# Kernel optimization log

Measured on AMD Instinct MI355X. Metric: run time of the kernel, lower is better.

Reference implementation:

```python
import jax, jax.numpy as jnp
import numpy as np

N_RES = 8192
N_IN = 128
BATCH = 16
RES_NNZ = int(0.1 * N_RES * N_RES)  # 6710886
IN_NNZ = int(0.1 * N_RES * N_IN)    # 104857
LEAK = 0.9


def spmm_coo(vals, rows, cols, inputs, n_out):
    """COO SpMM: out[b, r] = sum_{n: rows[n]==r} vals[n] * inputs[b, cols[n]].
    Equivalent to (coo_matmat(vals, rows, cols, inputs.T, shape=(n_out, F)).T)."""
    contrib = vals[:, None] * inputs.T[cols]  # [nnz, B]
    return jax.ops.segment_sum(contrib, rows, num_segments=n_out).T  # [B, n_out]


def leaky_erf(z, state, a=LEAK):
    return (1.0 - a) * state + a * jax.scipy.special.erf(z)


def setup_inputs() -> dict:
    key = jax.random.key(0)
    ks = jax.random.split(key, 10)
    return {
        "state": jax.random.normal(ks[0], (BATCH, N_RES), jnp.float32),
        "x": jax.random.normal(ks[1], (BATCH, N_IN), jnp.float32),
        "res_vals": jax.random.normal(ks[2], (RES_NNZ,), jnp.float32),
        "res_rows": jax.random.randint(ks[3], (RES_NNZ,), 0, N_RES, jnp.int32),
        "res_cols": jax.random.randint(ks[4], (RES_NNZ,), 0, N_RES, jnp.int32),
        "res_bias": jax.random.normal(ks[5], (N_RES,), jnp.float32),
        "in_vals": jax.random.normal(ks[6], (IN_NNZ,), jnp.float32),
        "in_rows": jax.random.randint(ks[7], (IN_NNZ,), 0, N_RES, jnp.int32),
        "in_cols": jax.random.randint(ks[8], (IN_NNZ,), 0, N_IN, jnp.int32),
        "in_bias": jax.random.normal(ks[9], (N_RES,), jnp.float32),
    }


def reference(state, x, res_vals, res_rows, res_cols, res_bias,
              in_vals, in_rows, in_cols, in_bias):
    z_res = spmm_coo(res_vals, res_rows, res_cols, state, N_RES) + res_bias
    z_in = spmm_coo(in_vals, in_rows, in_cols, x, N_RES) + in_bias
    return leaky_erf(z_in + z_res, state)
```

## Files before the change

### kernel.cpp

```cpp
#include <hip/hip_runtime.h>
#include <math.h>

#define N_RES 8192
#define N_IN  128
#define BATCH 16
#define LEAK  0.9f

#define NBK    128
#define CAP1B  55296
#define CHUNK1 8192
#define CHUNK2 4096
#define SB2    14
#define TBLK   128


#define OFF_SRCT 0
#define OFF_BCUR (1u << 20)
#define OFF_Z    (2u << 20)
#define OFF_E1   (8u << 20)
#define REQ_A    ((size_t)OFF_E1 + (size_t)NBK * CAP1B * 8)

__global__ __launch_bounds__(1024, 8) void pass1_fused(
    const float* __restrict__ state,
    const float* __restrict__ x,
    const float* __restrict__ vres, const int* __restrict__ rres,
    const int* __restrict__ cres, int nres, int nbres,
    const float* __restrict__ vin, const int* __restrict__ rin,
    const int* __restrict__ cin, int nin, int nchunks,
    float* __restrict__ srcT,
    float* __restrict__ z,
    uint2* __restrict__ e1,
    int* __restrict__ bcur) {
  int tid = threadIdx.x;

  if (blockIdx.x >= nchunks) {
    int idx0 = (blockIdx.x - nchunks) * 1024 + tid;
    const int stride = TBLK * 1024;
    for (int i = idx0; i < N_RES * BATCH; i += stride) {
      int b = i >> 13;
      int r = i & (N_RES - 1);
      srcT[r * BATCH + b] = state[i];
      z[i] = 0.0f;
    }
    for (int i = idx0; i < N_IN * BATCH; i += stride) {
      int b = i >> 7;
      int c = i & (N_IN - 1);
      srcT[(N_RES + c) * BATCH + b] = x[i];
    }
    return;
  }

  const float* vals; const int* rows; const int* cols;
  int nnz, col_off, base;
  if (blockIdx.x < nbres) {
    vals = vres; rows = rres; cols = cres; nnz = nres; col_off = 0;
    base = blockIdx.x * CHUNK1;
  } else {
    vals = vin; rows = rin; cols = cin; nnz = nin; col_off = N_RES;
    base = (blockIdx.x - nbres) * CHUNK1;
  }

  __shared__ uint2 stg[CHUNK1];
  __shared__ int hist[NBK];
  __shared__ int lbase[NBK];
  __shared__ int gbase[NBK];
  __shared__ int wsum[2];
  int wave = tid >> 6, lane = tid & 63;

  if (tid < NBK) hist[tid] = 0;
  __syncthreads();

  int n = nnz - base;
  if (n > CHUNK1) n = CHUNK1;

  uint2 ent[8];
  int lp[8];
  unsigned msk = 0;
#pragma unroll
  for (int g = 0; g < 2; ++g) {
    int i0 = (g * 1024 + tid) * 4;
    if (i0 + 3 < n) {
      int4 r4 = *(const int4*)(rows + base + i0);
      int4 c4 = *(const int4*)(cols + base + i0);
      float4 v4 = *(const float4*)(vals + base + i0);
      int rr_[4] = {r4.x, r4.y, r4.z, r4.w};
      int cc_[4] = {c4.x, c4.y, c4.z, c4.w};
      float vv_[4] = {v4.x, v4.y, v4.z, v4.w};
#pragma unroll
      for (int j = 0; j < 4; ++j) {
        int e = g * 4 + j;
        ent[e] = make_uint2(__float_as_uint(vv_[j]),
                            ((unsigned)rr_[j] << 14) |
                                (unsigned)(cc_[j] + col_off));
        msk |= 1u << e;
        lp[e] = atomicAdd(&hist[rr_[j] >> 6], 1);
      }
    } else {
#pragma unroll
      for (int j = 0; j < 4; ++j) {
        int e = g * 4 + j, i = i0 + j;
        if (i < n) {
          int r = rows[base + i];
          int c = cols[base + i] + col_off;
          float v = vals[base + i];
          ent[e] = make_uint2(__float_as_uint(v),
                              ((unsigned)r << 14) | (unsigned)c);
          msk |= 1u << e;
          lp[e] = atomicAdd(&hist[r >> 6], 1);
        }
      }
    }
  }
  __syncthreads();

  int h = 0, v = 0;
  if (tid < NBK) {
    h = hist[tid];
    v = h;
#pragma unroll
    for (int d = 1; d < 64; d <<= 1) {
      int t = __shfl_up(v, d);
      if (lane >= d) v += t;
    }
    if (lane == 63) wsum[wave] = v;
  }
  __syncthreads();
  if (tid < NBK) {
    int off = (wave == 1) ? wsum[0] : 0;
    lbase[tid] = off + v - h;
    gbase[tid] = h ? atomicAdd(&bcur[tid], h) : 0;
  }
  __syncthreads();
#pragma unroll
  for (int e = 0; e < 8; ++e) {
    if (msk & (1u << e)) {
      int b = (int)(ent[e].y >> 20);
      stg[lbase[b] + lp[e]] = ent[e];
    }
  }
  __syncthreads();
  for (int i = tid; i < n; i += 1024) {
    uint2 ld = stg[i];
    int b = (int)(ld.y >> 20);
    int p = gbase[b] + (i - lbase[b]);
    if (p < CAP1B) e1[(size_t)b * CAP1B + p] = ld;
  }
}

__global__ __launch_bounds__(512, 8) void pass2_accum(
    const uint2* __restrict__ e1,
    const int* __restrict__ bcur,
    const float* __restrict__ srcT,
    float* __restrict__ z) {
  int bucket = blockIdx.y;
  int ch = blockIdx.x;
  int tid = threadIdx.x;

  int cnt = bcur[bucket];
  if (cnt > CAP1B) cnt = CAP1B;
  int base = ch * CHUNK2;
  if (base >= cnt) return;
  int n = cnt - base;
  if (n > CHUNK2) n = CHUNK2;

  __shared__ int acc[64 * 17];
  for (int i = tid; i < 64 * 17; i += 512) acc[i] = 0;
  __syncthreads();

  const uint2* __restrict__ src = e1 + (size_t)bucket * CAP1B + base;
  int wave = tid >> 6, lane = tid & 63;
  int g = lane >> 2;
  int bq = lane & 3;
  const float4* __restrict__ s4 = (const float4*)srcT;

  int bw = wave * (CHUNK2 / 8);
  int lim = n - bw;
  if (lim > CHUNK2 / 8) lim = CHUNK2 / 8;
  for (int s = 0; s < lim; s += 32) {
    int i1 = bw + s + g;
    int i2 = bw + s + 16 + g;
    int c1 = (i1 < n) ? i1 : n - 1;
    int c2 = (i2 < n) ? i2 : n - 1;
    uint2 eA = src[c1];
    uint2 eB = src[c2];
    float4 sA = s4[(int)(eA.y & 16383u) * 4 + bq];
    float4 sB = s4[(int)(eB.y & 16383u) * 4 + bq];
    float vA = (i1 < n) ? __uint_as_float(eA.x) * 65536.f : 0.0f;
    float vB = (i2 < n) ? __uint_as_float(eB.x) * 65536.f : 0.0f;
    int aA = (int)((eA.y >> 14) & 63u) * 17 + (bq << 2);
    int aB = (int)((eB.y >> 14) & 63u) * 17 + (bq << 2);
    atomicAdd(&acc[aA + 0], __float2int_rn(vA * sA.x));
    atomicAdd(&acc[aA + 1], __float2int_rn(vA * sA.y));
    atomicAdd(&acc[aA + 2], __float2int_rn(vA * sA.z));
    atomicAdd(&acc[aA + 3], __float2int_rn(vA * sA.w));
    atomicAdd(&acc[aB + 0], __float2int_rn(vB * sB.x));
    atomicAdd(&acc[aB + 1], __float2int_rn(vB * sB.y));
    atomicAdd(&acc[aB + 2], __float2int_rn(vB * sB.z));
    atomicAdd(&acc[aB + 3], __float2int_rn(vB * sB.w));
  }
  __syncthreads();
  for (int i = tid; i < 64 * BATCH; i += 512) {
    int rr = i >> 4, b = i & 15;
    float fv = (float)acc[rr * 17 + b] * (1.0f / 65536.f);
    unsafeAtomicAdd(&z[(size_t)(bucket * 64 + rr) * BATCH + b], fv);
  }
}

__global__ __launch_bounds__(256) void finalize_z(
    const float* __restrict__ z, const float* __restrict__ state,
    const float* __restrict__ res_bias, const float* __restrict__ in_bias,
    float* __restrict__ out) {
  int tid = blockIdx.x * 256 + threadIdx.x;
  if (tid >= BATCH * N_RES) return;
  int b = tid >> 13;
  int r = tid & (N_RES - 1);
  float zz = z[r * 16 + b] + res_bias[r] + in_bias[r];
  out[tid] = (1.0f - LEAK) * state[tid] + LEAK * erff(zz);
}

__global__ __launch_bounds__(256) void transpose_nb(
    const float* __restrict__ state, const float* __restrict__ x,
    float* __restrict__ srcT) {
  int tid = blockIdx.x * 256 + threadIdx.x;
  if (tid < N_RES * BATCH) {
    int b = tid >> 13;
    int r = tid & (N_RES - 1);
    srcT[r * BATCH + b] = state[tid];
  }
  if (tid < N_IN * BATCH) {
    int b = tid >> 7;
    int c = tid & (N_IN - 1);
    srcT[(N_RES + c) * BATCH + b] = x[tid];
  }
}

__global__ __launch_bounds__(256) void spmm_atomic(
    const float* __restrict__ vals, const int* __restrict__ rows,
    const int* __restrict__ cols, const float* __restrict__ srcT,
    int col_off, float* __restrict__ zz, int nnz) {
  int i = blockIdx.x * blockDim.x + threadIdx.x;
  if (i >= nnz) return;
  float v = vals[i];
  int r = rows[i];
  int c = cols[i] + col_off;
  const float4* __restrict__ sp = (const float4*)(srcT + c * BATCH);
  float* zr = zz + r * BATCH;
#pragma unroll
  for (int qq = 0; qq < 4; ++qq) {
    float4 s = sp[qq];
    unsafeAtomicAdd(zr + qq * 4 + 0, v * s.x);
    unsafeAtomicAdd(zr + qq * 4 + 1, v * s.y);
    unsafeAtomicAdd(zr + qq * 4 + 2, v * s.z);
    unsafeAtomicAdd(zr + qq * 4 + 3, v * s.w);
  }
}

extern "C" void kernel_launch(void* const* d_in, const int* in_sizes, int n_in,
                              void* d_out, int out_size, void* d_ws, size_t ws_size,
                              hipStream_t stream) {
  const float* state    = (const float*)d_in[0];
  const float* x        = (const float*)d_in[1];
  const float* res_vals = (const float*)d_in[2];
  const int*   res_rows = (const int*)d_in[3];
  const int*   res_cols = (const int*)d_in[4];
  const float* res_bias = (const float*)d_in[5];
  const float* in_vals  = (const float*)d_in[6];
  const int*   in_rows  = (const int*)d_in[7];
  const int*   in_cols  = (const int*)d_in[8];
  const float* in_bias  = (const float*)d_in[9];

  const int res_nnz = in_sizes[2];
  const int in_nnz  = in_sizes[6];

  char* ws = (char*)d_ws;
  float* srcT = (float*)(ws + OFF_SRCT);
  float* z    = (float*)(ws + OFF_Z);
  float* out = (float*)d_out;

  if (ws_size >= REQ_A) {
    int* bcur = (int*)(ws + OFF_BCUR);
    uint2* e1 = (uint2*)(ws + OFF_E1);
    int nbres = (res_nnz + CHUNK1 - 1) / CHUNK1;
    int nbin  = (in_nnz + CHUNK1 - 1) / CHUNK1;
    int nchunks = nbres + nbin;

    hipMemsetAsync(bcur, 0, NBK * sizeof(int), stream);

    pass1_fused<<<nchunks + TBLK, 1024, 0, stream>>>(
        state, x, res_vals, res_rows, res_cols, res_nnz, nbres,
        in_vals, in_rows, in_cols, in_nnz, nchunks, srcT, z, e1, bcur);

    pass2_accum<<<dim3(SB2, NBK), 512, 0, stream>>>(e1, bcur, srcT, z);

    finalize_z<<<512, 256, 0, stream>>>(z, state, res_bias, in_bias, out);
  } else {
    hipMemsetAsync(z, 0, N_RES * BATCH * sizeof(float), stream);
    transpose_nb<<<512, 256, 0, stream>>>(state, x, srcT);
    spmm_atomic<<<(res_nnz + 255) / 256, 256, 0, stream>>>(
        res_vals, res_rows, res_cols, srcT, 0, z, res_nnz);
    spmm_atomic<<<(in_nnz + 255) / 256, 256, 0, stream>>>(
        in_vals, in_rows, in_cols, srcT, N_RES, z, in_nnz);
    finalize_z<<<512, 256, 0, stream>>>(z, state, res_bias, in_bias, out);
  }
}
```

Measured before the change: 185.9 us.

## Fuse all passes into one cooperative persistent kernel with grid syncs

Replaces the memset plus three kernel launches with a single cooperative kernel of 512 blocks that runs transpose/zero, bucket scatter, bucket accumulation and finalize as phases separated by grid-wide syncs. The goal is to remove launch gaps and the separate memset. In exchange, pass1 now runs in a grid-stride loop over chunks with fewer blocks, pass2 runs with 1024-thread blocks over a persistent loop, and three grid barriers are added. Co-residency of 512 blocks of 1024 threads must hold, otherwise the code falls back to the old path.

```diff
diff --git a/kernel.cpp b/kernel.cpp
--- a/kernel.cpp
+++ b/kernel.cpp
@@ -1,5 +1,8 @@
 #include <hip/hip_runtime.h>
+#include <hip/hip_cooperative_groups.h>
 #include <math.h>
+
+namespace cg = cooperative_groups;
 
 #define N_RES 8192
 #define N_IN  128
@@ -12,6 +15,7 @@
 #define CHUNK2 4096
 #define SB2    14
 #define TBLK   128
+#define GRID_B 512
 
 
 #define OFF_SRCT 0
@@ -20,7 +24,7 @@
 #define OFF_E1   (8u << 20)
 #define REQ_A    ((size_t)OFF_E1 + (size_t)NBK * CAP1B * 8)
 
-__global__ __launch_bounds__(1024, 8) void pass1_fused(
+__global__ __launch_bounds__(1024, 8) void fused_all(
     const float* __restrict__ state,
     const float* __restrict__ x,
     const float* __restrict__ vres, const int* __restrict__ rres,
@@ -30,7 +34,213 @@
     float* __restrict__ srcT,
     float* __restrict__ z,
     uint2* __restrict__ e1,
-    int* __restrict__ bcur) {
+    int* __restrict__ bcur,
+    const float* __restrict__ res_bias,
+    const float* __restrict__ in_bias,
+    float* __restrict__ out) {
+  cg::grid_group grid = cg::this_grid();
+  int tid = threadIdx.x;
+  int bid = blockIdx.x;
+
+  __shared__ __align__(16) char smem[CHUNK1 * 8 + 1536];
+
+  {
+    int idx = bid * 1024 + tid;
+    if (idx < N_RES * BATCH) {
+      int b = idx >> 13;
+      int r = idx & (N_RES - 1);
+      srcT[r * BATCH + b] = state[idx];
+      z[idx] = 0.0f;
+    }
+    if (idx < N_IN * BATCH) {
+      int b = idx >> 7;
+      int c = idx & (N_IN - 1);
+      srcT[(N_RES + c) * BATCH + b] = x[idx];
+    }
+    if (idx < NBK) bcur[idx] = 0;
+  }
+  grid.sync();
+
+  {
+    uint2* stg = (uint2*)smem;
+    int* hist  = (int*)(smem + CHUNK1 * 8);
+    int* lbase = (int*)(smem + CHUNK1 * 8 + 512);
+    int* gbase = (int*)(smem + CHUNK1 * 8 + 1024);
+    int* wsum  = (int*)(smem + CHUNK1 * 8 + 1528);
+    int wave = tid >> 6, lane = tid & 63;
+
+    for (int chk = bid; chk < nchunks; chk += GRID_B) {
+      const float* vals; const int* rows; const int* cols;
+      int nnz, col_off, base;
+      if (chk < nbres) {
+        vals = vres; rows = rres; cols = cres; nnz = nres; col_off = 0;
+        base = chk * CHUNK1;
+      } else {
+        vals = vin; rows = rin; cols = cin; nnz = nin; col_off = N_RES;
+        base = (chk - nbres) * CHUNK1;
+      }
+
+      if (tid < NBK) hist[tid] = 0;
+      __syncthreads();
+
+      int n = nnz - base;
+      if (n > CHUNK1) n = CHUNK1;
+
+      uint2 ent[8];
+      int lp[8];
+      unsigned msk = 0;
+#pragma unroll
+      for (int gg = 0; gg < 2; ++gg) {
+        int i0 = (gg * 1024 + tid) * 4;
+        if (i0 + 3 < n) {
+          int4 r4 = *(const int4*)(rows + base + i0);
+          int4 c4 = *(const int4*)(cols + base + i0);
+          float4 v4 = *(const float4*)(vals + base + i0);
+          int rr_[4] = {r4.x, r4.y, r4.z, r4.w};
+          int cc_[4] = {c4.x, c4.y, c4.z, c4.w};
+          float vv_[4] = {v4.x, v4.y, v4.z, v4.w};
+#pragma unroll
+          for (int j = 0; j < 4; ++j) {
+            int e = gg * 4 + j;
+            ent[e] = make_uint2(__float_as_uint(vv_[j]),
+                                ((unsigned)rr_[j] << 14) |
+                                    (unsigned)(cc_[j] + col_off));
+            msk |= 1u << e;
+            lp[e] = atomicAdd(&hist[rr_[j] >> 6], 1);
+          }
+        } else {
+#pragma unroll
+          for (int j = 0; j < 4; ++j) {
+            int e = gg * 4 + j, i = i0 + j;
+            if (i < n) {
+              int r = rows[base + i];
+              int c = cols[base + i] + col_off;
+              float v = vals[base + i];
+              ent[e] = make_uint2(__float_as_uint(v),
+                                  ((unsigned)r << 14) | (unsigned)c);
+              msk |= 1u << e;
+              lp[e] = atomicAdd(&hist[r >> 6], 1);
+            }
+          }
+        }
+      }
+      __syncthreads();
+
+      int h = 0, v = 0;
+      if (tid < NBK) {
+        h = hist[tid];
+        v = h;
+#pragma unroll
+        for (int d = 1; d < 64; d <<= 1) {
+          int t = __shfl_up(v, d);
+          if (lane >= d) v += t;
+        }
+        if (lane == 63) wsum[wave] = v;
+      }
+      __syncthreads();
+      if (tid < NBK) {
+        int off = (wave == 1) ? wsum[0] : 0;
+        lbase[tid] = off + v - h;
+        gbase[tid] = h ? atomicAdd(&bcur[tid], h) : 0;
+      }
+      __syncthreads();
+#pragma unroll
+      for (int e = 0; e < 8; ++e) {
+        if (msk & (1u << e)) {
+          int b = (int)(ent[e].y >> 20);
+          stg[lbase[b] + lp[e]] = ent[e];
+        }
+      }
+      __syncthreads();
+      for (int i = tid; i < n; i += 1024) {
+        uint2 ld = stg[i];
+        int b = (int)(ld.y >> 20);
+        int p = gbase[b] + (i - lbase[b]);
+        if (p < CAP1B) e1[(size_t)b * CAP1B + p] = ld;
+      }
+    }
+  }
+  grid.sync();
+
+  {
+    int* acc = (int*)smem;
+    int wave = tid >> 6, lane = tid & 63;
+    int g = lane >> 2;
+    int bq = lane & 3;
+    const float4* __restrict__ s4 = (const float4*)srcT;
+
+    for (int u = bid; u < SB2 * NBK; u += GRID_B) {
+      int bucket = u & (NBK - 1);
+      int ch = u >> 7;
+      int cnt = bcur[bucket];
+      if (cnt > CAP1B) cnt = CAP1B;
+      int base = ch * CHUNK2;
+      int n = cnt - base;
+      if (n < 0) n = 0;
+      if (n > CHUNK2) n = CHUNK2;
+
+      for (int i = tid; i < 64 * 17; i += 1024) acc[i] = 0;
+      __syncthreads();
+
+      if (n > 0) {
+        const uint2* __restrict__ src = e1 + (size_t)bucket * CAP1B + base;
+        int bw = wave * (CHUNK2 / 16);
+        int lim = n - bw;
+        if (lim < 0) lim = 0;
+        if (lim > CHUNK2 / 16) lim = CHUNK2 / 16;
+        for (int s = 0; s < lim; s += 32) {
+          int i1 = bw + s + g;
+          int i2 = bw + s + 16 + g;
+          int c1 = (i1 < n) ? i1 : n - 1;
+          int c2 = (i2 < n) ? i2 : n - 1;
+          uint2 eA = src[c1];
+          uint2 eB = src[c2];
+          float4 sA = s4[(int)(eA.y & 16383u) * 4 + bq];
+          float4 sB = s4[(int)(eB.y & 16383u) * 4 + bq];
+          float vA = (i1 < n) ? __uint_as_float(eA.x) * 65536.f : 0.0f;
+          float vB = (i2 < n) ? __uint_as_float(eB.x) * 65536.f : 0.0f;
+          int aA = (int)((eA.y >> 14) & 63u) * 17 + (bq << 2);
+          int aB = (int)((eB.y >> 14) & 63u) * 17 + (bq << 2);
+          atomicAdd(&acc[aA + 0], __float2int_rn(vA * sA.x));
+          atomicAdd(&acc[aA + 1], __float2int_rn(vA * sA.y));
+          atomicAdd(&acc[aA + 2], __float2int_rn(vA * sA.z));
+          atomicAdd(&acc[aA + 3], __float2int_rn(vA * sA.w));
+          atomicAdd(&acc[aB + 0], __float2int_rn(vB * sB.x));
+          atomicAdd(&acc[aB + 1], __float2int_rn(vB * sB.y));
+          atomicAdd(&acc[aB + 2], __float2int_rn(vB * sB.z));
+          atomicAdd(&acc[aB + 3], __float2int_rn(vB * sB.w));
+        }
+      }
+      __syncthreads();
+      if (n > 0 && tid < 64 * BATCH) {
+        int rr = tid >> 4, b = tid & 15;
+        float fv = (float)acc[rr * 17 + b] * (1.0f / 65536.f);
+        unsafeAtomicAdd(&z[(size_t)(bucket * 64 + rr) * BATCH + b], fv);
+      }
+      __syncthreads();
+    }
+  }
+  grid.sync();
+
+  {
+    int idx = bid * 1024 + tid;
+    if (idx < BATCH * N_RES) {
+      int b = idx >> 13;
+      int r = idx & (N_RES - 1);
+      float zz = z[r * 16 + b] + res_bias[r] + in_bias[r];
+      out[idx] = (1.0f - LEAK) * state[idx] + LEAK * erff(zz);
+    }
+  }
+}
+
+__global__ __launch_bounds__(1024, 8) void pass1_fused(
+    const float* __restrict__ state, const float* __restrict__ x,
+    const float* __restrict__ vres, const int* __restrict__ rres,
+    const int* __restrict__ cres, int nres, int nbres,
+    const float* __restrict__ vin, const int* __restrict__ rin,
+    const int* __restrict__ cin, int nin, int nchunks,
+    float* __restrict__ srcT, float* __restrict__ z,
+    uint2* __restrict__ e1, int* __restrict__ bcur) {
   int tid = threadIdx.x;
 
   if (blockIdx.x >= nchunks) {
@@ -148,10 +358,8 @@
 }
 
 __global__ __launch_bounds__(512, 8) void pass2_accum(
-    const uint2* __restrict__ e1,
-    const int* __restrict__ bcur,
-    const float* __restrict__ srcT,
-    float* __restrict__ z) {
+    const uint2* __restrict__ e1, const int* __restrict__ bcur,
+    const float* __restrict__ srcT, float* __restrict__ z) {
   int bucket = blockIdx.y;
   int ch = blockIdx.x;
   int tid = threadIdx.x;
@@ -275,7 +483,7 @@
   char* ws = (char*)d_ws;
   float* srcT = (float*)(ws + OFF_SRCT);
   float* z    = (float*)(ws + OFF_Z);
-  float* out = (float*)d_out;
+  float* out  = (float*)d_out;
 
   if (ws_size >= REQ_A) {
     int* bcur = (int*)(ws + OFF_BCUR);
@@ -284,15 +492,31 @@
     int nbin  = (in_nnz + CHUNK1 - 1) / CHUNK1;
     int nchunks = nbres + nbin;
 
-    hipMemsetAsync(bcur, 0, NBK * sizeof(int), stream);
-
-    pass1_fused<<<nchunks + TBLK, 1024, 0, stream>>>(
-        state, x, res_vals, res_rows, res_cols, res_nnz, nbres,
-        in_vals, in_rows, in_cols, in_nnz, nchunks, srcT, z, e1, bcur);
-
-    pass2_accum<<<dim3(SB2, NBK), 512, 0, stream>>>(e1, bcur, srcT, z);
-
-    finalize_z<<<512, 256, 0, stream>>>(z, state, res_bias, in_bias, out);
+    int coop = 0;
+    hipDeviceGetAttribute(&coop, hipDeviceAttributeCooperativeLaunch, 0);
+    hipError_t lerr = hipErrorUnknown;
+    if (coop) {
+      void* args[] = {
+          (void*)&state, (void*)&x,
+          (void*)&res_vals, (void*)&res_rows, (void*)&res_cols,
+          (void*)&res_nnz, (void*)&nbres,
+          (void*)&in_vals, (void*)&in_rows, (void*)&in_cols,
+          (void*)&in_nnz, (void*)&nchunks,
+          (void*)&srcT, (void*)&z, (void*)&e1, (void*)&bcur,
+          (void*)&res_bias, (void*)&in_bias, (void*)&out};
+      lerr = hipLaunchCooperativeKernel((const void*)fused_all,
+                                        dim3(GRID_B), dim3(1024),
+                                        args, 0, stream);
+    }
+    if (lerr != hipSuccess) {
+      (void)hipGetLastError();
+      hipMemsetAsync(bcur, 0, NBK * sizeof(int), stream);
+      pass1_fused<<<nchunks + TBLK, 1024, 0, stream>>>(
+          state, x, res_vals, res_rows, res_cols, res_nnz, nbres,
+          in_vals, in_rows, in_cols, in_nnz, nchunks, srcT, z, e1, bcur);
+      pass2_accum<<<dim3(SB2, NBK), 512, 0, stream>>>(e1, bcur, srcT, z);
+      finalize_z<<<512, 256, 0, stream>>>(z, state, res_bias, in_bias, out);
+    }
   } else {
     hipMemsetAsync(z, 0, N_RES * BATCH * sizeof(float), stream);
     transpose_nb<<<512, 256, 0, stream>>>(state, x, srcT);
```

Result: slower. 391.9 us (+110.8%).
